# Optimization experiments

Measured on AMD Instinct MI355X. Metric: run time of the kernel, lower is better.

The kernel has to match this reference:

```python
import jax, jax.numpy as jnp
import numpy as np

N = 50000   # nodes
E = 800000  # edges (before self-loops)
IN, HID, OUT = 128, 128, 64


def gcn_norm(edge_index, num_nodes):
    # add self loops with weight 1, then symmetric deg^-1/2 normalization
    loop = jnp.arange(num_nodes, dtype=edge_index.dtype)
    row = jnp.concatenate([edge_index[0], loop])
    col = jnp.concatenate([edge_index[1], loop])
    ew = jnp.ones(row.shape[0], dtype=jnp.float32)
    deg = jax.ops.segment_sum(ew, col, num_segments=num_nodes)
    dis = jnp.where(deg > 0, jax.lax.rsqrt(deg), 0.0)
    norm = dis[row] * ew * dis[col]
    return row, col, norm


def gcn_conv(x, row, col, norm, W, b):
    h = x @ W                                   # [N, F_out] dense GEMM
    msg = h[row] * norm[:, None]                # gather + scale over edges
    out = jax.ops.segment_sum(msg, col, num_segments=x.shape[0])  # scatter-add
    return out + b


def setup_inputs() -> dict:
    key = jax.random.key(0)
    k0, k1, k2, k3, k4, k5 = jax.random.split(key, 6)
    x = jax.random.normal(k0, (N, IN), dtype=jnp.float32)
    edge_index = jax.random.randint(k1, (2, E), 0, N, dtype=jnp.int32)
    # glorot-style init for linear weights, zeros for bias (PyG default)
    W1 = jax.random.normal(k2, (IN, HID), dtype=jnp.float32) * np.float32(np.sqrt(1.0 / IN))
    b1 = jnp.zeros((HID,), dtype=jnp.float32)
    W2 = jax.random.normal(k3, (HID, OUT), dtype=jnp.float32) * np.float32(np.sqrt(1.0 / HID))
    b2 = jnp.zeros((OUT,), dtype=jnp.float32)
    return {"x": x, "edge_index": edge_index, "W1": W1, "b1": b1, "W2": W2, "b2": b2}


def reference(x, edge_index, W1, b1, W2, b2):
    row, col, norm = gcn_norm(edge_index, x.shape[0])
    h = jax.nn.relu(gcn_conv(x, row, col, norm, W1, b1))
    # dropout is a no-op in eval mode (training=False)
    out = gcn_conv(h, row, col, norm, W2, b2)
    return out
```

## Files before the change

### kernel.cpp

```cpp
#include <hip/hip_runtime.h>
#include <hip/hip_fp16.h>


#define Nn 50000
#define Ne 800000
#define SCAN_B ((Nn + 1023) / 1024)
#define GT ((Nn + 63) / 64)
#define E2B ((Ne / 2 + 255) / 256)

using f16x8 = _Float16 __attribute__((ext_vector_type(8)));
using f32x4 = float __attribute__((ext_vector_type(4)));

__global__ __launch_bounds__(256) void k_gemm128_count(
    const float* __restrict__ X, const float* __restrict__ W,
    __half* __restrict__ H, const int2* __restrict__ col2,
    int* __restrict__ degi, ushort2* __restrict__ rank2) {
  __shared__ _Float16 Xs[64 * 136];
  __shared__ _Float16 Wts[128 * 136];

  if ((int)blockIdx.x >= GT) {
    int t = ((int)blockIdx.x - GT) * 256 + threadIdx.x;
    if (t < Ne / 2) {
      int2 c = col2[t];
      unsigned short r0 = (unsigned short)atomicAdd(&degi[c.x], 1);
      unsigned short r1 = (unsigned short)atomicAdd(&degi[c.y], 1);
      ushort2 rk; rk.x = r0; rk.y = r1;
      rank2[t] = rk;
    }
    return;
  }

  const int tid = threadIdx.x;
  const int base = blockIdx.x * 64;

  {
    for (int idx4 = tid; idx4 < 32 * 128; idx4 += 256) {
      int k = idx4 >> 5;
      int c = (idx4 & 31) * 4;
      float4 wv = ((const float4*)W)[idx4];
      Wts[(c + 0) * 136 + k] = (_Float16)wv.x;
      Wts[(c + 1) * 136 + k] = (_Float16)wv.y;
      Wts[(c + 2) * 136 + k] = (_Float16)wv.z;
      Wts[(c + 3) * 136 + k] = (_Float16)wv.w;
    }
  }
  {
    for (int u = tid; u < 64 * 16; u += 256) {
      int r = u >> 4, seg = u & 15;
      int node = base + r;
      if (node >= Nn) node = Nn - 1;
      const float4* xg = (const float4*)(X + (size_t)node * 128 + seg * 8);
      float4 x0 = xg[0], x1 = xg[1];
      f16x8 hv;
      hv[0] = (_Float16)x0.x; hv[1] = (_Float16)x0.y;
      hv[2] = (_Float16)x0.z; hv[3] = (_Float16)x0.w;
      hv[4] = (_Float16)x1.x; hv[5] = (_Float16)x1.y;
      hv[6] = (_Float16)x1.z; hv[7] = (_Float16)x1.w;
      *(f16x8*)&Xs[r * 136 + seg * 8] = hv;
    }
  }
  __syncthreads();

  const int w = tid >> 6, lane = tid & 63;
  const int quad = lane >> 4, mrow = lane & 15;

  f32x4 acc[8];
  #pragma unroll
  for (int ct = 0; ct < 8; ++ct) acc[ct] = (f32x4){0.f, 0.f, 0.f, 0.f};

  #pragma unroll
  for (int ko = 0; ko < 4; ++ko) {
    f16x8 av = *(const f16x8*)&Xs[(w * 16 + mrow) * 136 + ko * 32 + quad * 8];
    #pragma unroll
    for (int ct = 0; ct < 8; ++ct) {
      f16x8 bv = *(const f16x8*)&Wts[(ct * 16 + mrow) * 136 + ko * 32 + quad * 8];
      acc[ct] = __builtin_amdgcn_mfma_f32_16x16x32_f16(av, bv, acc[ct], 0, 0, 0);
    }
  }

  #pragma unroll
  for (int ct = 0; ct < 8; ++ct) {
    #pragma unroll
    for (int r = 0; r < 4; ++r) {
      int node = base + w * 16 + quad * 4 + r;
      if (node < Nn)
        H[(size_t)node * 128 + ct * 16 + mrow] = __float2half(acc[ct][r]);
    }
  }
}

__global__ __launch_bounds__(1024) void k_scan1(const int* __restrict__ degi,
                                                int* __restrict__ rowptr,
                                                float* __restrict__ dis,
                                                int* __restrict__ bsum) {
  __shared__ int wsum[16];
  int tid = threadIdx.x;
  int lane = tid & 63, wid = tid >> 6;
  int i = blockIdx.x * 1024 + tid;
  int v = (i < Nn) ? degi[i] : 0;
  if (i < Nn) dis[i] = rsqrtf((float)(v + 1));
  int incl = v;
  #pragma unroll
  for (int off = 1; off < 64; off <<= 1) {
    int t = __shfl_up(incl, off);
    if (lane >= off) incl += t;
  }
  if (lane == 63) wsum[wid] = incl;
  __syncthreads();
  if (wid == 0) {
    int wv = (lane < 16) ? wsum[lane] : 0;
    #pragma unroll
    for (int off = 1; off < 16; off <<= 1) {
      int t = __shfl_up(wv, off);
      if (lane >= off) wv += t;
    }
    if (lane < 16) wsum[lane] = wv;
  }
  __syncthreads();
  int woff = (wid > 0) ? wsum[wid - 1] : 0;
  if (i < Nn) rowptr[i] = woff + incl - v;
  if (tid == 0) bsum[blockIdx.x] = wsum[15];
}

__global__ __launch_bounds__(1024) void k_scan3(int* __restrict__ rowptr,
                                                const int* __restrict__ bsum,
                                                const float* __restrict__ W2,
                                                _Float16* __restrict__ W2h) {
  __shared__ int off_s;
  int tid = threadIdx.x;
  if (tid < 64) {
    int v = (tid < SCAN_B) ? bsum[tid] : 0;
    int incl = v;
    #pragma unroll
    for (int off = 1; off < 64; off <<= 1) {
      int t = __shfl_up(incl, off);
      if (tid >= off) incl += t;
    }
    if (tid == (int)blockIdx.x) off_s = incl - v;
    if (blockIdx.x == 0 && tid == SCAN_B - 1) rowptr[Nn] = incl;
  }
  __syncthreads();
  int i = blockIdx.x * 1024 + tid;
  if (i < Nn) rowptr[i] += off_s;
  if (blockIdx.x == 1) {
    for (int idx4 = tid; idx4 < 2048; idx4 += 1024) {
      int k = idx4 >> 4;
      int c = (idx4 & 15) * 4;
      float4 wv = ((const float4*)W2)[idx4];
      W2h[(c + 0) * 128 + k] = (_Float16)wv.x;
      W2h[(c + 1) * 128 + k] = (_Float16)wv.y;
      W2h[(c + 2) * 128 + k] = (_Float16)wv.z;
      W2h[(c + 3) * 128 + k] = (_Float16)wv.w;
    }
  }
}

__global__ __launch_bounds__(256) void k_fill(const int2* __restrict__ row2,
                                              const int2* __restrict__ col2,
                                              const int* __restrict__ rowptr,
                                              const ushort2* __restrict__ rank2,
                                              unsigned short* __restrict__ csr) {
  int t = blockIdx.x * 256 + threadIdx.x;
  if (t >= Ne / 2) return;
  int2 r = row2[t];
  int2 c = col2[t];
  ushort2 k = rank2[t];
  csr[rowptr[c.x] + (int)k.x] = (unsigned short)r.x;
  csr[rowptr[c.y] + (int)k.y] = (unsigned short)r.y;
}

__device__ __forceinline__ float2 h2f(unsigned int u) {
  return __half22float2(*(const __half2*)&u);
}

__global__ __launch_bounds__(256) void k_agg128_gemm64(
    const __half* __restrict__ H, const unsigned short* __restrict__ csr,
    const int* __restrict__ rowptr, const float* __restrict__ dis,
    const float* __restrict__ bias, const _Float16* __restrict__ W2h,
    __half* __restrict__ H2, int n) {
  __shared__ _Float16 Wts[64 * 136];
  __shared__ _Float16 Hs[16 * 136];

  const int tid = threadIdx.x;
  const int wid = tid >> 6, lane = tid & 63;
  const int sub = lane >> 4, fl = lane & 15;
  const int nb = wid * 4 + sub;
  const int v = blockIdx.x * 16 + nb;

  {
    const f16x8* Wq = (const f16x8*)W2h;
    for (int u = tid; u < 1024; u += 256) {
      int c = u >> 4, k8 = u & 15;
      *(f16x8*)&Wts[c * 136 + k8 * 8] = Wq[u];
    }
  }

  int s = rowptr[v], e = rowptr[v + 1];
  float d = dis[v];
  float sw = d * d;
  const uint4* Hq = (const uint4*)H;
  uint4 hv = Hq[(size_t)v * 16 + fl];
  float2 p0 = h2f(hv.x), p1 = h2f(hv.y), p2 = h2f(hv.z), p3 = h2f(hv.w);
  float a0 = p0.x * sw, a1 = p0.y * sw, a2 = p1.x * sw, a3 = p1.y * sw;
  float a4 = p2.x * sw, a5 = p2.y * sw, a6 = p3.x * sw, a7 = p3.y * sw;
  constexpr int D = 6;
  if (s < e) {
    int srcs[D];
    #pragma unroll
    for (int j = 0; j < D; ++j) {
      int idx = s + j;
      srcs[j] = csr[(idx < e) ? idx : (e - 1)];
    }
    for (int base = s; base < e; base += D) {
      uint4 q[D];
      float wd[D];
      #pragma unroll
      for (int j = 0; j < D; ++j) q[j] = Hq[(size_t)srcs[j] * 16 + fl];
      #pragma unroll
      for (int j = 0; j < D; ++j) wd[j] = dis[srcs[j]];
      int ns[D];
      #pragma unroll
      for (int j = 0; j < D; ++j) {
        int idx = base + D + j;
        ns[j] = csr[(idx < e) ? idx : (e - 1)];
      }
      #pragma unroll
      for (int j = 0; j < D; ++j) {
        float w = ((base + j) < e) ? wd[j] * d : 0.f;
        float2 t;
        t = h2f(q[j].x); a0 = fmaf(w, t.x, a0); a1 = fmaf(w, t.y, a1);
        t = h2f(q[j].y); a2 = fmaf(w, t.x, a2); a3 = fmaf(w, t.y, a3);
        t = h2f(q[j].z); a4 = fmaf(w, t.x, a4); a5 = fmaf(w, t.y, a5);
        t = h2f(q[j].w); a6 = fmaf(w, t.x, a6); a7 = fmaf(w, t.y, a7);
      }
      #pragma unroll
      for (int j = 0; j < D; ++j) srcs[j] = ns[j];
    }
  }
  {
    const float4* Bq = (const float4*)bias;
    float4 b0 = Bq[fl * 2], b1v = Bq[fl * 2 + 1];
    f16x8 hrow;
    hrow[0] = (_Float16)fmaxf(a0 + b0.x, 0.f);
    hrow[1] = (_Float16)fmaxf(a1 + b0.y, 0.f);
    hrow[2] = (_Float16)fmaxf(a2 + b0.z, 0.f);
    hrow[3] = (_Float16)fmaxf(a3 + b0.w, 0.f);
    hrow[4] = (_Float16)fmaxf(a4 + b1v.x, 0.f);
    hrow[5] = (_Float16)fmaxf(a5 + b1v.y, 0.f);
    hrow[6] = (_Float16)fmaxf(a6 + b1v.z, 0.f);
    hrow[7] = (_Float16)fmaxf(a7 + b1v.w, 0.f);
    *(f16x8*)&Hs[nb * 136 + fl * 8] = hrow;
  }
  __syncthreads();

  const int quad = lane >> 4, mrow = lane & 15;
  f32x4 acc = (f32x4){0.f, 0.f, 0.f, 0.f};
  #pragma unroll
  for (int ko = 0; ko < 4; ++ko) {
    f16x8 av = *(const f16x8*)&Hs[mrow * 136 + ko * 32 + quad * 8];
    f16x8 bv = *(const f16x8*)&Wts[(wid * 16 + mrow) * 136 + ko * 32 + quad * 8];
    acc = __builtin_amdgcn_mfma_f32_16x16x32_f16(av, bv, acc, 0, 0, 0);
  }
  #pragma unroll
  for (int r = 0; r < 4; ++r) {
    int node = blockIdx.x * 16 + quad * 4 + r;
    if (node < n)
      H2[(size_t)node * 64 + wid * 16 + mrow] = __float2half(acc[r]);
  }
}

__global__ __launch_bounds__(256) void k_agg64(const __half* __restrict__ H,
                                               const unsigned short* __restrict__ csr,
                                               const int* __restrict__ rowptr,
                                               const float* __restrict__ dis,
                                               const float* __restrict__ bias,
                                               float* __restrict__ Out, int n) {
  const int wid = threadIdx.x >> 6, lane = threadIdx.x & 63;
  const int sub = lane >> 4, fl = lane & 15;
  int v = blockIdx.x * 16 + wid * 4 + sub;
  if (v >= n) return;
  int s = rowptr[v], e = rowptr[v + 1];
  float d = dis[v];
  float sw = d * d;
  const uint2* Hq = (const uint2*)H;
  uint2 hv = Hq[(size_t)v * 16 + fl];
  float2 p0 = h2f(hv.x), p1 = h2f(hv.y);
  float a0 = p0.x * sw, a1 = p0.y * sw, a2 = p1.x * sw, a3 = p1.y * sw;
  constexpr int D = 8;
  if (s < e) {
    int srcs[D];
    #pragma unroll
    for (int j = 0; j < D; ++j) {
      int idx = s + j;
      srcs[j] = csr[(idx < e) ? idx : (e - 1)];
    }
    for (int base = s; base < e; base += D) {
      uint2 q[D];
      float wd[D];
      #pragma unroll
      for (int j = 0; j < D; ++j) q[j] = Hq[(size_t)srcs[j] * 16 + fl];
      #pragma unroll
      for (int j = 0; j < D; ++j) wd[j] = dis[srcs[j]];
      int ns[D];
      #pragma unroll
      for (int j = 0; j < D; ++j) {
        int idx = base + D + j;
        ns[j] = csr[(idx < e) ? idx : (e - 1)];
      }
      #pragma unroll
      for (int j = 0; j < D; ++j) {
        float w = ((base + j) < e) ? wd[j] * d : 0.f;
        float2 t;
        t = h2f(q[j].x); a0 = fmaf(w, t.x, a0); a1 = fmaf(w, t.y, a1);
        t = h2f(q[j].y); a2 = fmaf(w, t.x, a2); a3 = fmaf(w, t.y, a3);
      }
      #pragma unroll
      for (int j = 0; j < D; ++j) srcs[j] = ns[j];
    }
  }
  const float4* Bq = (const float4*)bias;
  float4 b = Bq[fl];
  float4 o = make_float4(a0 + b.x, a1 + b.y, a2 + b.z, a3 + b.w);
  ((float4*)(Out + (size_t)v * 64))[fl] = o;
}

extern "C" void kernel_launch(void* const* d_in, const int* in_sizes, int n_in,
                              void* d_out, int out_size, void* d_ws, size_t ws_size,
                              hipStream_t stream) {
  const float* x  = (const float*)d_in[0];
  const int*   ei = (const int*)d_in[1];
  const int*   row = ei;
  const int*   col = ei + Ne;
  const float* W1 = (const float*)d_in[2];
  const float* b1 = (const float*)d_in[3];
  const float* W2 = (const float*)d_in[4];
  const float* b2 = (const float*)d_in[5];
  float* out = (float*)d_out;

  char* ws = (char*)d_ws;
  size_t off = 0;
  auto alloc = [&](size_t bytes) -> void* {
    void* p = ws + off;
    off += (bytes + 255) & ~(size_t)255;
    return p;
  };
  int*    degi   = (int*)   alloc(Nn * sizeof(int));
  int*    rowptr = (int*)   alloc((Nn + 1) * sizeof(int));
  float*  dis    = (float*) alloc(Nn * sizeof(float));
  int*    bsum   = (int*)   alloc(64 * sizeof(int));
  unsigned short* rank = (unsigned short*)alloc((size_t)Ne * sizeof(unsigned short));
  unsigned short* csr  = (unsigned short*)alloc((size_t)Ne * sizeof(unsigned short));
  __half* H1     = (__half*)alloc((size_t)Nn * 128 * sizeof(__half));
  __half* H2     = (__half*)alloc((size_t)Nn * 64 * sizeof(__half));
  _Float16* W2h  = (_Float16*)alloc(64 * 128 * sizeof(_Float16));

  hipMemsetAsync(degi, 0, Nn * sizeof(int), stream);

  const int NGB = (Nn + 15) / 16;

  k_gemm128_count<<<GT + E2B, 256, 0, stream>>>(x, W1, H1, (const int2*)col,
                                                degi, (ushort2*)rank);
  k_scan1<<<SCAN_B, 1024, 0, stream>>>(degi, rowptr, dis, bsum);
  k_scan3<<<SCAN_B, 1024, 0, stream>>>(rowptr, bsum, W2, W2h);
  k_fill<<<E2B, 256, 0, stream>>>((const int2*)row, (const int2*)col, rowptr,
                                  (const ushort2*)rank, csr);
  k_agg128_gemm64<<<NGB, 256, 0, stream>>>(H1, csr, rowptr, dis, b1, W2h, H2, Nn);
  k_agg64<<<NGB, 256, 0, stream>>>(H2, csr, rowptr, dis, b2, out, Nn);
}
```

Baseline: 196.2 us.

## Precompute swizzled fp16 weights in prep kernel and fold edge counting into GEMM blocks

Adds a prep kernel that zeroes the degree array, replacing the memset, and converts W1/W2 once to fp16 in a row layout with XOR-swizzled 8-element chunks. GEMM blocks then copy the weights with plain vector loads instead of each block transposing fp32 W1. Each GEMM block also performs 512 edges of degree counting, so the separate count blocks go away. X rows are loaded straight into registers instead of staged through shared memory. This cuts per-block conversion work, shared-memory use and one launch, but the prep kernel adds a dependency and reorders the atomic work.

```diff
diff --git a/kernel.cpp b/kernel.cpp
--- a/kernel.cpp
+++ b/kernel.cpp
@@ -4,65 +4,95 @@
 
 #define Nn 50000
 #define Ne 800000
+#define NE2 (Ne / 2)
 #define SCAN_B ((Nn + 1023) / 1024)
 #define GT ((Nn + 63) / 64)
-#define E2B ((Ne / 2 + 255) / 256)
+#define EPB 512
 
 using f16x8 = _Float16 __attribute__((ext_vector_type(8)));
 using f32x4 = float __attribute__((ext_vector_type(4)));
 
-__global__ __launch_bounds__(256) void k_gemm128_count(
-    const float* __restrict__ X, const float* __restrict__ W,
+__global__ __launch_bounds__(256) void k_prep(const float* __restrict__ W1,
+                                              const float* __restrict__ W2,
+                                              _Float16* __restrict__ W1h,
+                                              _Float16* __restrict__ W2h,
+                                              int* __restrict__ degi) {
+  const int b = blockIdx.x, t = threadIdx.x;
+  if (b < 49) {
+    int i = b * 256 + t;
+    if (i < Nn / 4) ((int4*)degi)[i] = make_int4(0, 0, 0, 0);
+  } else if (b == 49) {
+    for (int i = 0; i < 8; ++i) {
+      int id = i * 256 + t;
+      int c = id & 127, k8 = id >> 7;
+      f16x8 hv;
+      #pragma unroll
+      for (int j = 0; j < 8; ++j) hv[j] = (_Float16)W1[(k8 * 8 + j) * 128 + c];
+      *(f16x8*)&W1h[c * 128 + ((k8 ^ (c & 7)) << 3)] = hv;
+    }
+  } else {
+    for (int i = 0; i < 4; ++i) {
+      int id = i * 256 + t;
+      int c = id & 63, k8 = id >> 6;
+      f16x8 hv;
+      #pragma unroll
+      for (int j = 0; j < 8; ++j) hv[j] = (_Float16)W2[(k8 * 8 + j) * 64 + c];
+      *(f16x8*)&W2h[c * 128 + ((k8 ^ (c & 7)) << 3)] = hv;
+    }
+  }
+}
+
+__global__ __launch_bounds__(256, 4) void k_gemm128_count(
+    const float* __restrict__ X, const _Float16* __restrict__ W1h,
     __half* __restrict__ H, const int2* __restrict__ col2,
     int* __restrict__ degi, ushort2* __restrict__ rank2) {
-  __shared__ _Float16 Xs[64 * 136];
-  __shared__ _Float16 Wts[128 * 136];
-
-  if ((int)blockIdx.x >= GT) {
-    int t = ((int)blockIdx.x - GT) * 256 + threadIdx.x;
-    if (t < Ne / 2) {
-      int2 c = col2[t];
-      unsigned short r0 = (unsigned short)atomicAdd(&degi[c.x], 1);
-      unsigned short r1 = (unsigned short)atomicAdd(&degi[c.y], 1);
-      ushort2 rk; rk.x = r0; rk.y = r1;
-      rank2[t] = rk;
-    }
-    return;
-  }
+  __shared__ _Float16 Wts[128 * 128];
 
   const int tid = threadIdx.x;
   const int base = blockIdx.x * 64;
 
   {
-    for (int idx4 = tid; idx4 < 32 * 128; idx4 += 256) {
-      int k = idx4 >> 5;
-      int c = (idx4 & 31) * 4;
-      float4 wv = ((const float4*)W)[idx4];
-      Wts[(c + 0) * 136 + k] = (_Float16)wv.x;
-      Wts[(c + 1) * 136 + k] = (_Float16)wv.y;
-      Wts[(c + 2) * 136 + k] = (_Float16)wv.z;
-      Wts[(c + 3) * 136 + k] = (_Float16)wv.w;
-    }
-  }
+    const f16x8* src = (const f16x8*)W1h;
+    f16x8* dst = (f16x8*)Wts;
+    #pragma unroll
+    for (int i = 0; i < 8; ++i) dst[i * 256 + tid] = src[i * 256 + tid];
+  }
+
   {
-    for (int u = tid; u < 64 * 16; u += 256) {
-      int r = u >> 4, seg = u & 15;
-      int node = base + r;
-      if (node >= Nn) node = Nn - 1;
-      const float4* xg = (const float4*)(X + (size_t)node * 128 + seg * 8);
-      float4 x0 = xg[0], x1 = xg[1];
-      f16x8 hv;
-      hv[0] = (_Float16)x0.x; hv[1] = (_Float16)x0.y;
-      hv[2] = (_Float16)x0.z; hv[3] = (_Float16)x0.w;
-      hv[4] = (_Float16)x1.x; hv[5] = (_Float16)x1.y;
-      hv[6] = (_Float16)x1.z; hv[7] = (_Float16)x1.w;
-      *(f16x8*)&Xs[r * 136 + seg * 8] = hv;
-    }
-  }
-  __syncthreads();
+    int i0 = blockIdx.x * EPB + tid;
+    int i1 = i0 + 256;
+    if (i0 < NE2) {
+      int2 c = col2[i0];
+      ushort2 rk;
+      rk.x = (unsigned short)atomicAdd(&degi[c.x], 1);
+      rk.y = (unsigned short)atomicAdd(&degi[c.y], 1);
+      rank2[i0] = rk;
+    }
+    if (i1 < NE2) {
+      int2 c = col2[i1];
+      ushort2 rk;
+      rk.x = (unsigned short)atomicAdd(&degi[c.x], 1);
+      rk.y = (unsigned short)atomicAdd(&degi[c.y], 1);
+      rank2[i1] = rk;
+    }
+  }
 
   const int w = tid >> 6, lane = tid & 63;
   const int quad = lane >> 4, mrow = lane & 15;
+  int anode = base + w * 16 + mrow;
+  if (anode >= Nn) anode = Nn - 1;
+  const float4* xg = (const float4*)(X + (size_t)anode * 128);
+  f16x8 av[4];
+  #pragma unroll
+  for (int ko = 0; ko < 4; ++ko) {
+    float4 x0 = xg[ko * 8 + quad * 2];
+    float4 x1 = xg[ko * 8 + quad * 2 + 1];
+    av[ko][0] = (_Float16)x0.x; av[ko][1] = (_Float16)x0.y;
+    av[ko][2] = (_Float16)x0.z; av[ko][3] = (_Float16)x0.w;
+    av[ko][4] = (_Float16)x1.x; av[ko][5] = (_Float16)x1.y;
+    av[ko][6] = (_Float16)x1.z; av[ko][7] = (_Float16)x1.w;
+  }
+  __syncthreads();
 
   f32x4 acc[8];
   #pragma unroll
@@ -70,11 +100,11 @@
 
   #pragma unroll
   for (int ko = 0; ko < 4; ++ko) {
-    f16x8 av = *(const f16x8*)&Xs[(w * 16 + mrow) * 136 + ko * 32 + quad * 8];
     #pragma unroll
     for (int ct = 0; ct < 8; ++ct) {
-      f16x8 bv = *(const f16x8*)&Wts[(ct * 16 + mrow) * 136 + ko * 32 + quad * 8];
-      acc[ct] = __builtin_amdgcn_mfma_f32_16x16x32_f16(av, bv, acc[ct], 0, 0, 0);
+      int c = ct * 16 + mrow;
+      f16x8 bv = *(const f16x8*)&Wts[c * 128 + (((ko * 4 + quad) ^ (c & 7)) << 3)];
+      acc[ct] = __builtin_amdgcn_mfma_f32_16x16x32_f16(av[ko], bv, acc[ct], 0, 0, 0);
     }
   }
 
@@ -123,9 +153,7 @@
 }
 
 __global__ __launch_bounds__(1024) void k_scan3(int* __restrict__ rowptr,
-                                                const int* __restrict__ bsum,
-                                                const float* __restrict__ W2,
-                                                _Float16* __restrict__ W2h) {
+                                                const int* __restrict__ bsum) {
   __shared__ int off_s;
   int tid = threadIdx.x;
   if (tid < 64) {
@@ -142,17 +170,6 @@
   __syncthreads();
   int i = blockIdx.x * 1024 + tid;
   if (i < Nn) rowptr[i] += off_s;
-  if (blockIdx.x == 1) {
-    for (int idx4 = tid; idx4 < 2048; idx4 += 1024) {
-      int k = idx4 >> 4;
-      int c = (idx4 & 15) * 4;
-      float4 wv = ((const float4*)W2)[idx4];
-      W2h[(c + 0) * 128 + k] = (_Float16)wv.x;
-      W2h[(c + 1) * 128 + k] = (_Float16)wv.y;
-      W2h[(c + 2) * 128 + k] = (_Float16)wv.z;
-      W2h[(c + 3) * 128 + k] = (_Float16)wv.w;
-    }
-  }
 }
 
 __global__ __launch_bounds__(256) void k_fill(const int2* __restrict__ row2,
@@ -161,7 +178,7 @@
                                               const ushort2* __restrict__ rank2,
                                               unsigned short* __restrict__ csr) {
   int t = blockIdx.x * 256 + threadIdx.x;
-  if (t >= Ne / 2) return;
+  if (t >= NE2) return;
   int2 r = row2[t];
   int2 c = col2[t];
   ushort2 k = rank2[t];
@@ -178,7 +195,7 @@
     const int* __restrict__ rowptr, const float* __restrict__ dis,
     const float* __restrict__ bias, const _Float16* __restrict__ W2h,
     __half* __restrict__ H2, int n) {
-  __shared__ _Float16 Wts[64 * 136];
+  __shared__ _Float16 Wts[64 * 128];
   __shared__ _Float16 Hs[16 * 136];
 
   const int tid = threadIdx.x;
@@ -188,11 +205,10 @@
   const int v = blockIdx.x * 16 + nb;
 
   {
-    const f16x8* Wq = (const f16x8*)W2h;
-    for (int u = tid; u < 1024; u += 256) {
-      int c = u >> 4, k8 = u & 15;
-      *(f16x8*)&Wts[c * 136 + k8 * 8] = Wq[u];
-    }
+    const f16x8* src = (const f16x8*)W2h;
+    f16x8* dst = (f16x8*)Wts;
+    #pragma unroll
+    for (int i = 0; i < 4; ++i) dst[i * 256 + tid] = src[i * 256 + tid];
   }
 
   int s = rowptr[v], e = rowptr[v + 1];
@@ -255,11 +271,12 @@
 
   const int quad = lane >> 4, mrow = lane & 15;
   f32x4 acc = (f32x4){0.f, 0.f, 0.f, 0.f};
+  const int c = wid * 16 + mrow;
   #pragma unroll
   for (int ko = 0; ko < 4; ++ko) {
-    f16x8 av = *(const f16x8*)&Hs[mrow * 136 + ko * 32 + quad * 8];
-    f16x8 bv = *(const f16x8*)&Wts[(wid * 16 + mrow) * 136 + ko * 32 + quad * 8];
-    acc = __builtin_amdgcn_mfma_f32_16x16x32_f16(av, bv, acc, 0, 0, 0);
+    f16x8 avx = *(const f16x8*)&Hs[mrow * 136 + ko * 32 + quad * 8];
+    f16x8 bv = *(const f16x8*)&Wts[c * 128 + (((ko * 4 + quad) ^ (c & 7)) << 3)];
+    acc = __builtin_amdgcn_mfma_f32_16x16x32_f16(avx, bv, acc, 0, 0, 0);
   }
   #pragma unroll
   for (int r = 0; r < 4; ++r) {
@@ -352,17 +369,18 @@
   unsigned short* csr  = (unsigned short*)alloc((size_t)Ne * sizeof(unsigned short));
   __half* H1     = (__half*)alloc((size_t)Nn * 128 * sizeof(__half));
   __half* H2     = (__half*)alloc((size_t)Nn * 64 * sizeof(__half));
+  _Float16* W1h  = (_Float16*)alloc(128 * 128 * sizeof(_Float16));
   _Float16* W2h  = (_Float16*)alloc(64 * 128 * sizeof(_Float16));
 
-  hipMemsetAsync(degi, 0, Nn * sizeof(int), stream);
-
   const int NGB = (Nn + 15) / 16;
-
-  k_gemm128_count<<<GT + E2B, 256, 0, stream>>>(x, W1, H1, (const int2*)col,
-                                                degi, (ushort2*)rank);
+  const int E1B = (NE2 + 255) / 256;
+
+  k_prep<<<51, 256, 0, stream>>>(W1, W2, W1h, W2h, degi);
+  k_gemm128_count<<<GT, 256, 0, stream>>>(x, W1h, H1, (const int2*)col,
+                                          degi, (ushort2*)rank);
   k_scan1<<<SCAN_B, 1024, 0, stream>>>(degi, rowptr, dis, bsum);
-  k_scan3<<<SCAN_B, 1024, 0, stream>>>(rowptr, bsum, W2, W2h);
-  k_fill<<<E2B, 256, 0, stream>>>((const int2*)row, (const int2*)col, rowptr,
+  k_scan3<<<SCAN_B, 1024, 0, stream>>>(rowptr, bsum);
+  k_fill<<<E1B, 256, 0, stream>>>((const int2*)row, (const int2*)col, rowptr,
                                   (const ushort2*)rank, csr);
   k_agg128_gemm64<<<NGB, 256, 0, stream>>>(H1, csr, rowptr, dis, b1, W2h, H2, Nn);
   k_agg64<<<NGB, 256, 0, stream>>>(H2, csr, rowptr, dis, b2, out, Nn);
```

Result: faster. 186.5 us (-5.0%).
